# Kernel tuning notes

Measured on AMD Instinct MI355X. Metric: run time of the kernel, lower is better.

The kernel has to match this reference:

```python
import jax, jax.numpy as jnp
import numpy as np

T, N, H, DIN = 128, 256, 512, 255  # inputs last dim = DIN + 1 (trailing action channel)
PACK = H + 5  # packed state: a(1), loc(1), scale(1), v(1), h(H), p(1)


def setup_inputs() -> dict:
    key = jax.random.key(0)
    ks = jax.random.split(key, 12)
    f32 = jnp.float32
    def rn(k, shape, scale):
        return jax.random.normal(k, shape, dtype=f32) * scale
    si, sh = 1.0 / np.sqrt(DIN), 1.0 / np.sqrt(H)
    return {
        "inputs": jax.random.normal(ks[0], (T, N, DIN + 1), dtype=f32),
        "hx": rn(ks[1], (1, N, PACK), 0.1),
        "eps": jax.random.normal(ks[2], (T, N, 1), dtype=f32),
        "Wih": rn(ks[3], (3 * H, DIN), si),
        "Whh": rn(ks[4], (3 * H, H), sh),
        "bih": jnp.zeros((3 * H,), f32),
        "bhh": jnp.zeros((3 * H,), f32),
        "Wa0": rn(ks[5], (H, H), sh), "ba0": jnp.zeros((H,), f32),
        "Wa1": rn(ks[6], (H, H), sh), "ba1": jnp.zeros((H,), f32),
        "Wloc": rn(ks[7], (1, H), sh), "bloc": jnp.zeros((1,), f32),
        "logstd": jnp.zeros((1,), f32),
        "Wc0": rn(ks[8], (H, H), sh), "bc0": jnp.zeros((H,), f32),
        "Wc1": rn(ks[9], (H, H), sh), "bc1": jnp.zeros((H,), f32),
        "Wv": rn(ks[10], (1, H), sh), "bv": jnp.zeros((1,), f32),
    }


def _forward(inputs, hx, eps, Wih, Whh, bih, bhh, Wa0, ba0, Wa1, ba1,
             Wloc, bloc, logstd, Wc0, bc0, Wc1, bc1, Wv, bv):
    inputs = jax.lax.stop_gradient(inputs)  # module calls inputs.detach()
    obs, actions = inputs[..., :DIN], inputs[..., DIN:]
    hx0 = hx[0]                       # [N, PACK] after squeeze_(0)
    h0 = hx0[:, 4:4 + H]              # initial GRU hidden state
    p = hx0[:, H + 4:H + 5]           # [N,1], passed through unchanged

    def step(h, x_t):
        # PyTorch GRU cell math
        gi = x_t @ Wih.T + bih        # [N, 3H]
        gh = h @ Whh.T + bhh          # [N, 3H]
        ir, iz, in_ = jnp.split(gi, 3, axis=-1)
        hr, hz, hn = jnp.split(gh, 3, axis=-1)
        r = jax.nn.sigmoid(ir + hr)
        z = jax.nn.sigmoid(iz + hz)
        n = jnp.tanh(in_ + r * hn)
        h_new = (1.0 - z) * n + z * h
        return h_new, h_new

    _, hs = jax.lax.scan(step, h0, obs)  # [T, N, H]; hn == h for 1-layer unidir GRU

    def mlp2(x, W0, b0, W1, b1):
        return jnp.tanh(jnp.tanh(x @ W0.T + b0) @ W1.T + b1)

    # heads don't feed back into the recurrence -> apply to all timesteps at once
    loc = mlp2(hs, Wa0, ba0, Wa1, ba1) @ Wloc.T + bloc        # [T, N, 1]
    scale = jnp.broadcast_to(jnp.exp(logstd), loc.shape)      # DiagGaussian scale
    v = mlp2(hs, Wc0, bc0, Wc1, bc1) @ Wv.T + bv              # [T, N, 1]

    # sample_new: replace entries of A where actions < 0 with dist.sample()
    sample = jax.lax.stop_gradient(loc + scale * eps)         # .sample() is non-differentiable
    a = jnp.where(actions < 0, sample, actions)

    p_full = jnp.broadcast_to(p, (T, N, 1))
    # pack() order follows RecurrentState fields: a, loc, scale, v, h, p
    return jnp.concatenate([a, loc, scale, v, hs, p_full], axis=-1)  # [T, N, PACK]


def reference(inputs, hx, eps, Wih, Whh, bih, bhh, Wa0, ba0, Wa1, ba1,
              Wloc, bloc, logstd, Wc0, bc0, Wc1, bc1, Wv, bv):
    packed = _forward(inputs, hx, eps, Wih, Whh, bih, bhh, Wa0, ba0, Wa1, ba1,
                      Wloc, bloc, logstd, Wc0, bc0, Wc1, bc1, Wv, bv)
    return (packed, packed[-1:])
```

## Files before the change

### kernel.cpp

```cpp
#include <hip/hip_runtime.h>

typedef unsigned short u16;
typedef unsigned long long u64;
typedef __bf16 bf16x8 __attribute__((ext_vector_type(8)));
typedef float f32x4 __attribute__((ext_vector_type(4)));

#define T_STEPS 128
#define NB 256
#define HDIM 512
#define DIN_ 255
#define PACK_ 517
#define TN 32768

__device__ __forceinline__ float b2f(u16 u) {
    union { unsigned int i; float f; } v; v.i = ((unsigned int)u) << 16; return v.f;
}
__device__ __forceinline__ u16 f2b(float f) {
    union { float f; unsigned int i; } v; v.f = f;
    unsigned int r = v.i + 0x7FFFu + ((v.i >> 16) & 1u);
    return (u16)(r >> 16);
}
__device__ __forceinline__ float sigm(float x) { return 1.f / (1.f + __expf(-x)); }
__device__ __forceinline__ float ftanh(float x) { return 2.f * sigm(2.f * x) - 1.f; }

__device__ __forceinline__ bf16x8 ldx4(const u16* p) {
    f32x4 t;
    asm volatile("global_load_dwordx4 %0, %1, off" : "=v"(t) : "v"(p) : "memory");
    union { f32x4 f; bf16x8 b; } u; u.f = t; return u.b;
}
#define WAIT_VMCNT(N) asm volatile("s_waitcnt vmcnt(" #N ")" ::: "memory")
#define WAIT_LGKM0    asm volatile("s_waitcnt lgkmcnt(0)" ::: "memory")

template<int DO_TANH, int K, int MT>
__global__ __launch_bounds__(256) void gemm_bt(const u16* __restrict__ A,
                                               const u16* __restrict__ B,
                                               const float* __restrict__ bias,
                                               u16* __restrict__ C, int N) {
    __shared__ u16 lds[64 * K];
    int n0 = blockIdx.x * 64;
    int w = threadIdx.x >> 6, l = threadIdx.x & 63;
    int la = l & 15, lb = l >> 4;
    for (int idx = threadIdx.x; idx < 8 * K; idx += 256) {
        int kq = idx >> 6, row = idx & 63;
        *(bf16x8*)(lds + (size_t)idx * 8) =
            *(const bf16x8*)(B + (size_t)(n0 + row) * K + kq * 8);
    }
    __syncthreads();
    const u16* bq[4];
    #pragma unroll
    for (int c = 0; c < 4; ++c) bq[c] = lds + ((size_t)lb * 64 + 16 * c + la) * 8;

    for (int mt = 0; mt < MT; ++mt) {
        int m0 = (blockIdx.y * MT + mt) * 64;
        int mw = m0 + 16 * w;
        const u16* Ap = A + (size_t)(mw + la) * K + 8 * lb;
        f32x4 acc[4] = {};
        #pragma unroll
        for (int k0 = 0; k0 < K; k0 += 32) {
            bf16x8 a = *(const bf16x8*)(Ap + k0);
            #pragma unroll
            for (int c = 0; c < 4; ++c)
                acc[c] = __builtin_amdgcn_mfma_f32_16x16x32_bf16(
                    a, *(const bf16x8*)(bq[c] + (size_t)k0 * 64), acc[c], 0, 0, 0);
        }
        #pragma unroll
        for (int c = 0; c < 4; ++c) {
            int n = n0 + 16 * c + la;
            float bv = bias[n];
            #pragma unroll
            for (int r = 0; r < 4; ++r) {
                int m = mw + 4 * lb + r;
                float v = acc[c][r] + bv;
                if (DO_TANH) v = ftanh(v);
                C[(size_t)m * N + n] = f2b(v);
            }
        }
    }
}

__global__ __launch_bounds__(256, 1) void gru_persist(
    const u16* __restrict__ h0b, const float* __restrict__ hx,
    const u16* __restrict__ whh_b, const float* __restrict__ bhh,
    const u16* __restrict__ gi_b,
    u16* __restrict__ hs_b, unsigned int* __restrict__ bar) {
    extern __shared__ u16 lds[];
    __shared__ unsigned s_locv;
    const int tid = threadIdx.x;
    const int bid = blockIdx.x;
    const int g = bid & 7, s = bid >> 3;
    const int ks = s * 32, m0 = g * 32;
    const int w = tid >> 6, l = tid & 63;
    const int la = l & 15, lb = l >> 4;
    const int rw = w >> 1, cw = w & 1;
    const int mw = m0 + 16 * rw;
    const int kc = ks + 16 * cw;

    unsigned myx;
    asm volatile("s_getreg_b32 %0, hwreg(HW_REG_XCC_ID)" : "=s"(myx));
    myx = (myx & 15u) + 1u;
    unsigned int* tbl = bar + 8192;
    if (tid == 0)
        __hip_atomic_fetch_add(tbl + bid, myx, __ATOMIC_RELAXED,
                               __HIP_MEMORY_SCOPE_AGENT);

    for (int idx = tid; idx < 6144; idx += 256) {
        int kq = idx / 96, row = idx - kq * 96;
        int gg = row >> 5, rr = row & 31;
        *(bf16x8*)(lds + (size_t)idx * 8) =
            *(const bf16x8*)(whh_b + (size_t)(gg * HDIM + ks + rr) * HDIM + kq * 8);
    }
    const u16* bq[3];
    #pragma unroll
    for (int c = 0; c < 3; ++c)
        bq[c] = lds + (size_t)(lb * 96 + c * 32 + 16 * cw + la) * 8;
    float bh[3];
    #pragma unroll
    for (int gg = 0; gg < 3; ++gg) bh[gg] = bhh[gg * HDIM + kc + la];
    float hp[4];
    #pragma unroll
    for (int r = 0; r < 4; ++r)
        hp[r] = hx[(size_t)(mw + 4 * lb + r) * PACK_ + 4 + kc + la];

    if (tid == 0) {
        unsigned vals[16];
        int guard = 0;
        bool ok;
        do {
            ok = true;
            #pragma unroll
            for (int k = 0; k < 16; ++k) {
                vals[k] = __hip_atomic_fetch_add(tbl + g + 8 * k, 0u,
                                                 __ATOMIC_RELAXED,
                                                 __HIP_MEMORY_SCOPE_AGENT);
                ok = ok && (vals[k] != 0u);
            }
            if (!ok) __builtin_amdgcn_s_sleep(8);
        } while (!ok && ++guard < (1 << 16));
        unsigned lv = ok ? 1u : 0u;
        #pragma unroll
        for (int k = 1; k < 16; ++k) lv &= (unsigned)(vals[k] == vals[0]);
        s_locv = lv;
    }
    u16* packbuf = lds + 49152 + w * 256;
    __syncthreads();
    const bool loc = (s_locv != 0);
    unsigned int* myline = bar + (g * 16 + s) * 64;
    unsigned int* pline  = bar + (g * 16 + (l & 15)) * 64;

    for (int t = 0; t < T_STEPS; ++t) {
        const u16* gi_t = gi_b + (size_t)t * NB * 3 * HDIM;

        u16 giv[3][4];
        #pragma unroll
        for (int r = 0; r < 4; ++r) {
            const u16* gp = gi_t + (size_t)(mw + 4 * lb + r) * 1536 + kc + la;
            #pragma unroll
            for (int gg = 0; gg < 3; ++gg) giv[gg][r] = gp[gg * HDIM];
        }

        if (t > 0) {
            if (w == 0) {
                int guard = 0, delay = 32;
                for (;;) {
                    bool okl = true;
                    if (l < 16) {
                        unsigned v;
                        if (loc)
                            asm volatile(
                                "global_atomic_add %0, %1, %2, off sc0\n\t"
                                "s_waitcnt vmcnt(0)"
                                : "=v"(v) : "v"(pline), "v"(0u) : "memory");
                        else
                            v = __hip_atomic_fetch_add(pline, 0u, __ATOMIC_RELAXED,
                                                       __HIP_MEMORY_SCOPE_AGENT);
                        okl = ((int)v >= t);
                    }
                    if (__all(okl) || ++guard > (1 << 14)) break;
                    float z = (float)delay;
                    for (int q = 0; q < delay; ++q)
                        z = __builtin_fmaf(z, 1.0000001f, 0.0625f);
                    asm volatile("" :: "v"(z));
                    delay = delay < 2048 ? delay * 2 : 2048;
                }
            }
            __syncthreads();
            asm volatile("" ::: "memory");
        }

        const u16* Ap = (t ? hs_b + (size_t)(t - 1) * NB * HDIM : h0b)
                        + (size_t)(mw + la) * HDIM + 8 * lb;
        bf16x8 a[16];
        #pragma unroll
        for (int kk = 0; kk < 16; ++kk) a[kk] = ldx4(Ap + 32 * kk);

        f32x4 acc[3] = {};
        WAIT_VMCNT(8);
        __builtin_amdgcn_sched_barrier(0);
        #pragma unroll
        for (int kk = 0; kk < 8; ++kk) {
            #pragma unroll
            for (int c = 0; c < 3; ++c)
                acc[c] = __builtin_amdgcn_mfma_f32_16x16x32_bf16(
                    a[kk], *(const bf16x8*)(bq[c] + (size_t)kk * 3072), acc[c], 0, 0, 0);
        }
        WAIT_VMCNT(0);
        __builtin_amdgcn_sched_barrier(0);
        #pragma unroll
        for (int kk = 8; kk < 16; ++kk) {
            #pragma unroll
            for (int c = 0; c < 3; ++c)
                acc[c] = __builtin_amdgcn_mfma_f32_16x16x32_bf16(
                    a[kk], *(const bf16x8*)(bq[c] + (size_t)kk * 3072), acc[c], 0, 0, 0);
        }

        float hnewv[4];
        #pragma unroll
        for (int r = 0; r < 4; ++r) {
            float rr2 = sigm(b2f(giv[0][r]) + acc[0][r] + bh[0]);
            float zz  = sigm(b2f(giv[1][r]) + acc[1][r] + bh[1]);
            float nn  = ftanh(b2f(giv[2][r]) + rr2 * (acc[2][r] + bh[2]));
            float hnew = (1.f - zz) * nn + zz * hp[r];
            hp[r] = hnew;
            hnewv[r] = hnew;
        }

        #pragma unroll
        for (int r = 0; r < 4; ++r) {
            float nbv = __shfl_xor(hnewv[r], 1, 64);
            if (!(la & 1)) {
                unsigned pk = (unsigned)f2b(hnewv[r]) | ((unsigned)f2b(nbv) << 16);
                *(unsigned*)(packbuf + (4 * lb + r) * 16 + la) = pk;
            }
        }
        WAIT_LGKM0;
        __builtin_amdgcn_sched_barrier(0);
        u16* hs_t = hs_b + (size_t)t * NB * HDIM;
        if (l < 32) {
            bf16x8 hv = *(const bf16x8*)(packbuf + (l >> 1) * 16 + 8 * (l & 1));
            union { bf16x8 b; f32x4 f; } u; u.b = hv;
            u16* sp = hs_t + (size_t)(mw + (l >> 1)) * HDIM + kc + 8 * (l & 1);
            if (loc) asm volatile("global_store_dwordx4 %0, %1, off"
                                  :: "v"(sp), "v"(u.f) : "memory");
            else     asm volatile("global_store_dwordx4 %0, %1, off sc0 sc1"
                                  :: "v"(sp), "v"(u.f) : "memory");
        }
        WAIT_VMCNT(0);
        __syncthreads();
        if (t < T_STEPS - 1 && tid == 0) {
            if (loc)
                asm volatile("global_atomic_add %0, %1, off"
                             :: "v"(myline), "v"(1u) : "memory");
            else
                __hip_atomic_fetch_add(myline, 1u, __ATOMIC_RELAXED,
                                       __HIP_MEMORY_SCOPE_AGENT);
        }
    }
}

__global__ void expand_h(const u16* __restrict__ hs, float* __restrict__ out) {
    int idx = blockIdx.x * 256 + threadIdx.x;
    if (idx >= TN * 256) return;
    int m = idx >> 8, kk = (idx & 255) * 2;
    unsigned pk = *(const unsigned*)(hs + (size_t)m * HDIM + kk);
    float* o = out + (size_t)m * PACK_ + 4 + kk;
    o[0] = b2f((u16)(pk & 0xFFFFu));
    o[1] = b2f((u16)(pk >> 16));
}

__global__ __launch_bounds__(256) void head_dot(const u16* __restrict__ X,
                                                const u16* __restrict__ W,
                                                const float* __restrict__ b,
                                                float* __restrict__ out, int off) {
    int wid = (int)((blockIdx.x * blockDim.x + threadIdx.x) >> 6);
    int l = threadIdx.x & 63;
    if (wid >= TN) return;
    bf16x8 xv = *(const bf16x8*)(X + (size_t)wid * HDIM + 8 * l);
    bf16x8 wv = *(const bf16x8*)(W + 8 * l);
    float s = 0.f;
    #pragma unroll
    for (int j = 0; j < 8; ++j) s += (float)xv[j] * (float)wv[j];
    #pragma unroll
    for (int d = 32; d; d >>= 1) s += __shfl_down(s, d, 64);
    if (l == 0) out[(size_t)wid * PACK_ + off] = s + b[0];
}

__global__ void prep_w(const float* __restrict__ Wih, const float* __restrict__ Whh,
                       const float* __restrict__ Wa0, const float* __restrict__ Wa1,
                       const float* __restrict__ Wloc, const float* __restrict__ Wc0,
                       const float* __restrict__ Wc1, const float* __restrict__ Wv,
                       const float* __restrict__ hx,
                       u16* Wih_b, u16* Whh_b, u16* Wa0_b, u16* Wa1_b,
                       u16* Wloc_b, u16* Wc0_b, u16* Wc1_b, u16* Wv_b,
                       float* h0f, u16* h0b) {
    int i = blockIdx.x * 256 + threadIdx.x;
    if (i < 1536 * 256) { int r = i >> 8, c = i & 255;
        Wih_b[i] = (c < DIN_) ? f2b(Wih[r * DIN_ + c]) : (u16)0; return; }
    i -= 1536 * 256;
    if (i < 1536 * 512) { Whh_b[i] = f2b(Whh[i]); return; } i -= 1536 * 512;
    if (i < 512 * 512) { Wa0_b[i] = f2b(Wa0[i]); return; } i -= 512 * 512;
    if (i < 512 * 512) { Wa1_b[i] = f2b(Wa1[i]); return; } i -= 512 * 512;
    if (i < 512 * 512) { Wc0_b[i] = f2b(Wc0[i]); return; } i -= 512 * 512;
    if (i < 512 * 512) { Wc1_b[i] = f2b(Wc1[i]); return; } i -= 512 * 512;
    if (i < 512) { Wloc_b[i] = f2b(Wloc[i]); return; } i -= 512;
    if (i < 512) { Wv_b[i] = f2b(Wv[i]); return; } i -= 512;
    if (i < NB * HDIM) { int n = i >> 9, k = i & 511;
        float v = hx[n * PACK_ + 4 + k]; h0f[i] = v; h0b[i] = f2b(v); return; }
}

__global__ void prep_obs(const float* __restrict__ in, u16* __restrict__ obs) {
    int idx = blockIdx.x * 256 + threadIdx.x;
    if (idx >= TN * 32) return;
    int m = idx >> 5, j = idx & 31;
    const float* src = in + (size_t)m * 256 + 8 * j;
    union { u16 s[8]; uint4 u; } t;
    #pragma unroll
    for (int q = 0; q < 8; ++q) t.s[q] = f2b(src[q]);
    if (j == 31) t.s[7] = 0;
    *(uint4*)(obs + (size_t)m * 256 + 8 * j) = t.u;
}

__global__ void finalize_out(const float* __restrict__ in, const float* __restrict__ eps,
                             const float* __restrict__ hx, const float* __restrict__ logstd,
                             float* __restrict__ out) {
    int m = blockIdx.x * 256 + threadIdx.x;
    if (m >= TN) return;
    int n = m & (NB - 1);
    float scale = __expf(logstd[0]);
    float loc = out[(size_t)m * PACK_ + 1];
    float act = in[(size_t)m * 256 + DIN_];
    float a = (act < 0.f) ? (loc + scale * eps[m]) : act;
    out[(size_t)m * PACK_ + 0] = a;
    out[(size_t)m * PACK_ + 2] = scale;
    out[(size_t)m * PACK_ + PACK_ - 1] = hx[n * PACK_ + PACK_ - 1];
}

__global__ void tail_copy(float* __restrict__ out) {
    int i = blockIdx.x * 256 + threadIdx.x;
    if (i >= NB * PACK_) return;
    out[(size_t)T_STEPS * NB * PACK_ + i] = out[(size_t)(T_STEPS - 1) * NB * PACK_ + i];
}

extern "C" void kernel_launch(void* const* d_in, const int* in_sizes, int n_in,
                              void* d_out, int out_size, void* d_ws, size_t ws_size,
                              hipStream_t stream) {
    const float* inputs = (const float*)d_in[0];
    const float* hx     = (const float*)d_in[1];
    const float* eps    = (const float*)d_in[2];
    const float* Wih    = (const float*)d_in[3];
    const float* Whh    = (const float*)d_in[4];
    const float* bih    = (const float*)d_in[5];
    const float* bhh    = (const float*)d_in[6];
    const float* Wa0    = (const float*)d_in[7];
    const float* ba0    = (const float*)d_in[8];
    const float* Wa1    = (const float*)d_in[9];
    const float* ba1    = (const float*)d_in[10];
    const float* Wloc   = (const float*)d_in[11];
    const float* bloc   = (const float*)d_in[12];
    const float* logstd = (const float*)d_in[13];
    const float* Wc0    = (const float*)d_in[14];
    const float* bc0    = (const float*)d_in[15];
    const float* Wc1    = (const float*)d_in[16];
    const float* bc1    = (const float*)d_in[17];
    const float* Wv     = (const float*)d_in[18];
    const float* bv     = (const float*)d_in[19];
    float* out = (float*)d_out;
    char* ws = (char*)d_ws;

    const size_t o_gi   = 0;
    const size_t o_buf0 = 0;
    const size_t o_buf1 = 33554432;
    const size_t o_hs   = 100663296;
    const size_t o_obs  = o_hs + 33554432;
    const size_t o_whh  = o_obs + 16777216;
    const size_t o_wih  = o_whh + 1572864;
    const size_t o_wa0  = o_wih + 786432;
    const size_t o_wa1  = o_wa0 + 524288;
    const size_t o_wc0  = o_wa1 + 524288;
    const size_t o_wc1  = o_wc0 + 524288;
    const size_t o_wloc = o_wc1 + 524288;
    const size_t o_wv   = o_wloc + 1024;
    const size_t o_h0f  = o_wv + 1024;
    const size_t o_h0b  = o_h0f + 524288;
    const size_t o_bar  = o_h0b + 262144;
    const size_t NEED   = o_bar + 36864;
    if (ws_size < NEED) return;

    u16*   gi_b   = (u16*)(ws + o_gi);
    u16*   buf0   = (u16*)(ws + o_buf0);
    u16*   buf1   = (u16*)(ws + o_buf1);
    u16*   hs_b   = (u16*)(ws + o_hs);
    u16*   obs_b  = (u16*)(ws + o_obs);
    u16*   whh_b  = (u16*)(ws + o_whh);
    u16*   wih_b  = (u16*)(ws + o_wih);
    u16*   wa0_b  = (u16*)(ws + o_wa0);
    u16*   wa1_b  = (u16*)(ws + o_wa1);
    u16*   wc0_b  = (u16*)(ws + o_wc0);
    u16*   wc1_b  = (u16*)(ws + o_wc1);
    u16*   wloc_b = (u16*)(ws + o_wloc);
    u16*   wv_b   = (u16*)(ws + o_wv);
    float* h0f    = (float*)(ws + o_h0f);
    u16*   h0b    = (u16*)(ws + o_h0b);
    unsigned int* bar = (unsigned int*)(ws + o_bar);

    static bool attr_set = false;
    if (!attr_set) {
        hipFuncSetAttribute((const void*)gru_persist,
                            hipFuncAttributeMaxDynamicSharedMemorySize, 102400);
        attr_set = true;
    }

    hipMemsetAsync(bar, 0, 36864, stream);

    prep_w<<<9220, 256, 0, stream>>>(Wih, Whh, Wa0, Wa1, Wloc, Wc0, Wc1, Wv, hx,
                                     wih_b, whh_b, wa0_b, wa1_b, wloc_b, wc0_b, wc1_b, wv_b,
                                     h0f, h0b);
    prep_obs<<<4096, 256, 0, stream>>>(inputs, obs_b);

    gemm_bt<0, 256, 8><<<dim3(24, 64), 256, 0, stream>>>(obs_b, wih_b, bih, gi_b, 1536);

    gru_persist<<<128, 256, 102400, stream>>>(h0b, hx, whh_b, bhh, gi_b, hs_b, bar);

    expand_h<<<32768, 256, 0, stream>>>(hs_b, out);

    gemm_bt<1, 512, 8><<<dim3(8, 64), 256, 0, stream>>>(hs_b, wa0_b, ba0, buf0, 512);
    gemm_bt<1, 512, 8><<<dim3(8, 64), 256, 0, stream>>>(buf0, wa1_b, ba1, buf1, 512);
    head_dot<<<8192, 256, 0, stream>>>(buf1, wloc_b, bloc, out, 1);
    gemm_bt<1, 512, 8><<<dim3(8, 64), 256, 0, stream>>>(hs_b, wc0_b, bc0, buf0, 512);
    gemm_bt<1, 512, 8><<<dim3(8, 64), 256, 0, stream>>>(buf0, wc1_b, bc1, buf1, 512);
    head_dot<<<8192, 256, 0, stream>>>(buf1, wv_b, bv, out, 3);

    finalize_out<<<128, 256, 0, stream>>>(inputs, eps, hx, logstd, out);
    tail_copy<<<518, 256, 0, stream>>>(out);
}
```

Measured before the change: 1.514 ms.

## Overlap actor/critic heads with GRU recurrence using extra persistent worker blocks

Launches 128 extra blocks alongside the persistent GRU blocks. They poll per-timestep progress counters, then compute the two-layer actor and critic MLPs, the heads, sampling and packed output for each finished timestep while the recurrence continues. If worker placement or co-residency checks fail, a fallback counter lets the original separate head kernels run, and they exit early otherwise. This aims to hide head compute behind the serial recurrence, at the cost of extra spin-polling traffic and extra blocks sharing the GPU with the latency-critical GRU. The worker GEMMs read weights straight from global memory with no LDS reuse.

```diff
diff --git a/kernel.cpp b/kernel.cpp
--- a/kernel.cpp
+++ b/kernel.cpp
@@ -35,7 +35,9 @@
 __global__ __launch_bounds__(256) void gemm_bt(const u16* __restrict__ A,
                                                const u16* __restrict__ B,
                                                const float* __restrict__ bias,
-                                               u16* __restrict__ C, int N) {
+                                               u16* __restrict__ C, int N,
+                                               const unsigned* __restrict__ skip) {
+    if (skip && *skip == 128u) return;
     __shared__ u16 lds[64 * K];
     int n0 = blockIdx.x * 64;
     int w = threadIdx.x >> 6, l = threadIdx.x & 63;
@@ -82,23 +84,185 @@
     const u16* __restrict__ h0b, const float* __restrict__ hx,
     const u16* __restrict__ whh_b, const float* __restrict__ bhh,
     const u16* __restrict__ gi_b,
-    u16* __restrict__ hs_b, unsigned int* __restrict__ bar) {
+    u16* __restrict__ hs_b, unsigned int* __restrict__ bar,
+    const u16* __restrict__ wa0_b, const float* __restrict__ ba0,
+    const u16* __restrict__ wa1_b, const float* __restrict__ ba1,
+    const u16* __restrict__ wloc_b, const float* __restrict__ bloc,
+    const u16* __restrict__ wc0_b, const float* __restrict__ bc0,
+    const u16* __restrict__ wc1_b, const float* __restrict__ bc1,
+    const u16* __restrict__ wv_b, const float* __restrict__ bv,
+    float* __restrict__ out, const float* __restrict__ eps,
+    const float* __restrict__ inputs, const float* __restrict__ logstd) {
     extern __shared__ u16 lds[];
     __shared__ unsigned s_locv;
+    __shared__ unsigned s_eng;
+    __shared__ int s_ok;
     const int tid = threadIdx.x;
     const int bid = blockIdx.x;
+    const int w = tid >> 6, l = tid & 63;
+    const int la = l & 15, lb = l >> 4;
+    unsigned int* wyes = bar + 8576;
+    unsigned int* wno  = bar + 8592;
+    unsigned int* wfin = bar + 8608;
+    unsigned int* tbl  = bar + 8192;
+
+    unsigned myx;
+    asm volatile("s_getreg_b32 %0, hwreg(HW_REG_XCC_ID)" : "=s"(myx));
+    myx = (myx & 15u) + 1u;
+
+    if (bid >= 128) {
+        const int j = bid - 128;
+        const int g = j & 7;
+        if (tid == 0) {
+            unsigned vals[16];
+            int guard = 0; bool ok;
+            do {
+                ok = true;
+                #pragma unroll
+                for (int k = 0; k < 16; ++k) {
+                    vals[k] = __hip_atomic_fetch_add(tbl + g + 8 * k, 0u,
+                                                     __ATOMIC_RELAXED,
+                                                     __HIP_MEMORY_SCOPE_AGENT);
+                    ok = ok && (vals[k] != 0u);
+                }
+                if (!ok) __builtin_amdgcn_s_sleep(8);
+            } while (!ok && ++guard < (1 << 16));
+            unsigned lv = ok ? 1u : 0u;
+            #pragma unroll
+            for (int k = 0; k < 16; ++k) lv &= (unsigned)(vals[k] == myx);
+            __hip_atomic_fetch_add(lv ? wyes : wno, 1u, __ATOMIC_RELAXED,
+                                   __HIP_MEMORY_SCOPE_AGENT);
+            guard = 0;
+            unsigned y, n;
+            for (;;) {
+                y = __hip_atomic_fetch_add(wyes, 0u, __ATOMIC_RELAXED,
+                                           __HIP_MEMORY_SCOPE_AGENT);
+                n = __hip_atomic_fetch_add(wno, 0u, __ATOMIC_RELAXED,
+                                           __HIP_MEMORY_SCOPE_AGENT);
+                if (y + n >= 128u || ++guard > (1 << 16)) break;
+                __builtin_amdgcn_s_sleep(8);
+            }
+            s_eng = (n == 0u && y == 128u) ? 1u : 0u;
+            s_ok = 1;
+        }
+        __syncthreads();
+        if (!s_eng) return;
+
+        u16* xh  = lds;
+        u16* xt0 = lds + 16384;
+        u16* xt1 = lds + 32768;
+        float* hsc = (float*)(lds + 49152);
+
+        for (int it = 0; it < 8; ++it) {
+            const int t = (j >> 3) + 16 * it;
+            if (w == 0) {
+                unsigned int* pl = bar + (g * 16 + (l & 15)) * 64;
+                int guard = 0;
+                for (;;) {
+                    bool okl = true;
+                    if (l < 16) {
+                        unsigned v;
+                        asm volatile("global_atomic_add %0, %1, %2, off sc0\n\t"
+                                     "s_waitcnt vmcnt(0)"
+                                     : "=v"(v) : "v"(pl), "v"(0u) : "memory");
+                        okl = (v >= (unsigned)(t + 1));
+                    }
+                    if (__all(okl)) break;
+                    if (++guard > (1 << 16)) { if (l == 0) s_ok = 0; break; }
+                    __builtin_amdgcn_s_sleep(16);
+                }
+            }
+            __syncthreads();
+            if (!s_ok) break;
+
+            const u16* hsp = hs_b + (size_t)t * NB * HDIM + (size_t)g * 32 * HDIM;
+            for (int i = tid; i < 2048; i += 256)
+                *(bf16x8*)(xh + (size_t)i * 8) = *(const bf16x8*)(hsp + (size_t)i * 8);
+            __syncthreads();
+
+            const int rw = w & 1, ch = w >> 1;
+            auto do_gemm = [&](const u16* X, const u16* Wm,
+                               const float* bias, u16* Y) {
+                bf16x8 a[16];
+                #pragma unroll
+                for (int kk = 0; kk < 16; ++kk)
+                    a[kk] = *(const bf16x8*)(X + (16 * rw + la) * 512 + 8 * lb + 32 * kk);
+                for (int c = 0; c < 16; ++c) {
+                    int n0 = 256 * ch + 16 * c;
+                    f32x4 acc = {};
+                    #pragma unroll
+                    for (int kk = 0; kk < 16; ++kk) {
+                        bf16x8 b = *(const bf16x8*)(Wm + (size_t)(n0 + la) * 512
+                                                    + 8 * lb + 32 * kk);
+                        acc = __builtin_amdgcn_mfma_f32_16x16x32_bf16(a[kk], b, acc, 0, 0, 0);
+                    }
+                    float bvv = bias[n0 + la];
+                    #pragma unroll
+                    for (int r = 0; r < 4; ++r)
+                        Y[(16 * rw + 4 * lb + r) * 512 + n0 + la] = f2b(ftanh(acc[r] + bvv));
+                }
+                __syncthreads();
+            };
+            auto do_head = [&](const u16* X, const u16* Wh,
+                               const float* bh_, float* dst) {
+                for (int rr = 0; rr < 8; ++rr) {
+                    int row = 8 * w + rr;
+                    bf16x8 xv = *(const bf16x8*)(X + row * 512 + 8 * l);
+                    bf16x8 wv = *(const bf16x8*)(Wh + 8 * l);
+                    float s2 = 0.f;
+                    #pragma unroll
+                    for (int q = 0; q < 8; ++q) s2 += (float)xv[q] * (float)wv[q];
+                    #pragma unroll
+                    for (int d = 32; d; d >>= 1) s2 += __shfl_down(s2, d, 64);
+                    if (l == 0) dst[row] = s2 + bh_[0];
+                }
+                __syncthreads();
+            };
+
+            do_gemm(xh, wa0_b, ba0, xt0);
+            do_gemm(xt0, wa1_b, ba1, xt1);
+            do_head(xt1, wloc_b, bloc, hsc);
+            do_gemm(xh, wc0_b, bc0, xt0);
+            do_gemm(xt0, wc1_b, bc1, xt1);
+            do_head(xt1, wv_b, bv, hsc + 32);
+
+            const int row = tid >> 3, part = tid & 7;
+            const int m = g * 32 + row;
+            float* o0 = out + (size_t)(t * NB + m) * PACK_;
+            float* o1 = out + (size_t)(T_STEPS * NB + m) * PACK_;
+            const int kb = part * 64;
+            for (int q = 0; q < 64; ++q) {
+                float hv = b2f(xh[row * 512 + kb + q]);
+                o0[4 + kb + q] = hv;
+                if (t == T_STEPS - 1) o1[4 + kb + q] = hv;
+            }
+            if (part == 0) {
+                float locv = hsc[row], vv2 = hsc[32 + row];
+                float scale = __expf(logstd[0]);
+                float act = inputs[(size_t)(t * NB + m) * 256 + DIN_];
+                float a2 = (act < 0.f) ? (locv + scale * eps[t * NB + m]) : act;
+                float pv = hx[(size_t)m * PACK_ + PACK_ - 1];
+                o0[0] = a2; o0[1] = locv; o0[2] = scale; o0[3] = vv2;
+                o0[PACK_ - 1] = pv;
+                if (t == T_STEPS - 1) {
+                    o1[0] = a2; o1[1] = locv; o1[2] = scale; o1[3] = vv2;
+                    o1[PACK_ - 1] = pv;
+                }
+            }
+            __syncthreads();
+        }
+        if (tid == 0 && s_ok)
+            __hip_atomic_fetch_add(wfin, 1u, __ATOMIC_RELAXED,
+                                   __HIP_MEMORY_SCOPE_AGENT);
+        return;
+    }
+
     const int g = bid & 7, s = bid >> 3;
     const int ks = s * 32, m0 = g * 32;
-    const int w = tid >> 6, l = tid & 63;
-    const int la = l & 15, lb = l >> 4;
     const int rw = w >> 1, cw = w & 1;
     const int mw = m0 + 16 * rw;
     const int kc = ks + 16 * cw;
 
-    unsigned myx;
-    asm volatile("s_getreg_b32 %0, hwreg(HW_REG_XCC_ID)" : "=s"(myx));
-    myx = (myx & 15u) + 1u;
-    unsigned int* tbl = bar + 8192;
     if (tid == 0)
         __hip_atomic_fetch_add(tbl + bid, myx, __ATOMIC_RELAXED,
                                __HIP_MEMORY_SCOPE_AGENT);
@@ -123,8 +287,7 @@
 
     if (tid == 0) {
         unsigned vals[16];
-        int guard = 0;
-        bool ok;
+        int guard = 0; bool ok;
         do {
             ok = true;
             #pragma unroll
@@ -246,7 +409,7 @@
         }
         WAIT_VMCNT(0);
         __syncthreads();
-        if (t < T_STEPS - 1 && tid == 0) {
+        if (tid == 0) {
             if (loc)
                 asm volatile("global_atomic_add %0, %1, off"
                              :: "v"(myline), "v"(1u) : "memory");
@@ -257,7 +420,9 @@
     }
 }
 
-__global__ void expand_h(const u16* __restrict__ hs, float* __restrict__ out) {
+__global__ void expand_h(const u16* __restrict__ hs, float* __restrict__ out,
+                         const unsigned* __restrict__ skip) {
+    if (*skip == 128u) return;
     int idx = blockIdx.x * 256 + threadIdx.x;
     if (idx >= TN * 256) return;
     int m = idx >> 8, kk = (idx & 255) * 2;
@@ -270,7 +435,9 @@
 __global__ __launch_bounds__(256) void head_dot(const u16* __restrict__ X,
                                                 const u16* __restrict__ W,
                                                 const float* __restrict__ b,
-                                                float* __restrict__ out, int off) {
+                                                float* __restrict__ out, int off,
+                                                const unsigned* __restrict__ skip) {
+    if (*skip == 128u) return;
     int wid = (int)((blockIdx.x * blockDim.x + threadIdx.x) >> 6);
     int l = threadIdx.x & 63;
     if (wid >= TN) return;
@@ -321,7 +488,9 @@
 
 __global__ void finalize_out(const float* __restrict__ in, const float* __restrict__ eps,
                              const float* __restrict__ hx, const float* __restrict__ logstd,
-                             float* __restrict__ out) {
+                             float* __restrict__ out,
+                             const unsigned* __restrict__ skip) {
+    if (*skip == 128u) return;
     int m = blockIdx.x * 256 + threadIdx.x;
     if (m >= TN) return;
     int n = m & (NB - 1);
@@ -334,7 +503,8 @@
     out[(size_t)m * PACK_ + PACK_ - 1] = hx[n * PACK_ + PACK_ - 1];
 }
 
-__global__ void tail_copy(float* __restrict__ out) {
+__global__ void tail_copy(float* __restrict__ out, const unsigned* __restrict__ skip) {
+    if (*skip == 128u) return;
     int i = blockIdx.x * 256 + threadIdx.x;
     if (i >= NB * PACK_) return;
     out[(size_t)T_STEPS * NB * PACK_ + i] = out[(size_t)(T_STEPS - 1) * NB * PACK_ + i];
@@ -401,6 +571,7 @@
     float* h0f    = (float*)(ws + o_h0f);
     u16*   h0b    = (u16*)(ws + o_h0b);
     unsigned int* bar = (unsigned int*)(ws + o_bar);
+    const unsigned* wfin = (const unsigned*)(ws + o_bar + 8608 * 4);
 
     static bool attr_set = false;
     if (!attr_set) {
@@ -416,19 +587,22 @@
                                      h0f, h0b);
     prep_obs<<<4096, 256, 0, stream>>>(inputs, obs_b);
 
-    gemm_bt<0, 256, 8><<<dim3(24, 64), 256, 0, stream>>>(obs_b, wih_b, bih, gi_b, 1536);
-
-    gru_persist<<<128, 256, 102400, stream>>>(h0b, hx, whh_b, bhh, gi_b, hs_b, bar);
-
-    expand_h<<<32768, 256, 0, stream>>>(hs_b, out);
-
-    gemm_bt<1, 512, 8><<<dim3(8, 64), 256, 0, stream>>>(hs_b, wa0_b, ba0, buf0, 512);
-    gemm_bt<1, 512, 8><<<dim3(8, 64), 256, 0, stream>>>(buf0, wa1_b, ba1, buf1, 512);
-    head_dot<<<8192, 256, 0, stream>>>(buf1, wloc_b, bloc, out, 1);
-    gemm_bt<1, 512, 8><<<dim3(8, 64), 256, 0, stream>>>(hs_b, wc0_b, bc0, buf0, 512);
-    gemm_bt<1, 512, 8><<<dim3(8, 64), 256, 0, stream>>>(buf0, wc1_b, bc1, buf1, 512);
-    head_dot<<<8192, 256, 0, stream>>>(buf1, wv_b, bv, out, 3);
-
-    finalize_out<<<128, 256, 0, stream>>>(inputs, eps, hx, logstd, out);
-    tail_copy<<<518, 256, 0, stream>>>(out);
-}
+    gemm_bt<0, 256, 8><<<dim3(24, 64), 256, 0, stream>>>(obs_b, wih_b, bih, gi_b,
+                                                         1536, nullptr);
+
+    gru_persist<<<256, 256, 102400, stream>>>(
+        h0b, hx, whh_b, bhh, gi_b, hs_b, bar,
+        wa0_b, ba0, wa1_b, ba1, wloc_b, bloc,
+        wc0_b, bc0, wc1_b, bc1, wv_b, bv,
+        out, eps, inputs, logstd);
+
+    expand_h<<<32768, 256, 0, stream>>>(hs_b, out, wfin);
+    gemm_bt<1, 512, 8><<<dim3(8, 64), 256, 0, stream>>>(hs_b, wa0_b, ba0, buf0, 512, wfin);
+    gemm_bt<1, 512, 8><<<dim3(8, 64), 256, 0, stream>>>(buf0, wa1_b, ba1, buf1, 512, wfin);
+    head_dot<<<8192, 256, 0, stream>>>(buf1, wloc_b, bloc, out, 1, wfin);
+    gemm_bt<1, 512, 8><<<dim3(8, 64), 256, 0, stream>>>(hs_b, wc0_b, bc0, buf0, 512, wfin);
+    gemm_bt<1, 512, 8><<<dim3(8, 64), 256, 0, stream>>>(buf0, wc1_b, bc1, buf1, 512, wfin);
+    head_dot<<<8192, 256, 0, stream>>>(buf1, wv_b, bv, out, 3, wfin);
+    finalize_out<<<128, 256, 0, stream>>>(inputs, eps, hx, logstd, out, wfin);
+    tail_copy<<<518, 256, 0, stream>>>(out, wfin);
+}
```

New measurement: 2.146 ms. 1.42x slower.
